# Kernel optimization log

Measured on AMD Instinct MI355X. Metric: run time of the kernel, lower is better.

The kernel has to match this reference:

```python
import jax, jax.numpy as jnp
import numpy as np

B = 2048          # graphs in dense batch
NPG = 64          # nodes per graph (molecules are small)
N = B * NPG       # 131072 total nodes
E = 524288        # directed edges, avg degree 4
D = 275           # dim_inner
L = 5             # layers_mp
NF = 9            # atom categorical features
V = 128           # per-feature vocab
BN_EPS = 1e-5


def setup_inputs() -> dict:
    key = jax.random.key(0)
    ks = jax.random.split(key, 8)
    return {
        "x_atoms": jax.random.randint(ks[0], (N, NF), 0, 119, dtype=jnp.int64),
        "edge_index": jax.random.randint(ks[1], (2, E), 0, N, dtype=jnp.int64),
        "atom_emb": jax.random.normal(ks[2], (NF, V, D), jnp.float32) * 0.1,
        "conv_W": jax.random.normal(ks[3], (L, D, D), jnp.float32) * (1.0 / np.sqrt(D)),
        "conv_b": jnp.zeros((L, D), jnp.float32),
        "bn_gamma": jnp.ones((L, D), jnp.float32),
        "bn_beta": jnp.zeros((L, D), jnp.float32),
        "post_W": jax.random.normal(ks[4], (D, D), jnp.float32) * (1.0 / np.sqrt(D)),
        "post_b": jnp.zeros((D,), jnp.float32),
    }


def reference(x_atoms, edge_index, atom_emb, conv_W, conv_b, bn_gamma, bn_beta, post_W, post_b):
    n = x_atoms.shape[0]
    # AtomEncoder: sum of per-feature embedding lookups -> [N, D]
    h = jax.vmap(lambda tab, idx: tab[idx], in_axes=(0, 1))(atom_emb, x_atoms).sum(0)

    # GCN normalization with self loops (shared across layers since graph is fixed)
    loops = jnp.arange(n, dtype=edge_index.dtype)
    row = jnp.concatenate([edge_index[0], loops])  # source
    col = jnp.concatenate([edge_index[1], loops])  # target (aggregation index)
    deg = jax.ops.segment_sum(jnp.ones_like(row, h.dtype), col, num_segments=n)
    dinv = jnp.where(deg > 0, jax.lax.rsqrt(jnp.maximum(deg, 1e-12)), 0.0)
    norm = dinv[row] * dinv[col]  # [E+N]

    for i in range(L):
        xw = h @ conv_W[i].T                                   # [N, D] linear (no bias yet)
        msg = norm[:, None] * xw[row]                          # gather + edge scaling
        agg = jax.ops.segment_sum(msg, col, num_segments=n) + conv_b[i]
        # BatchNorm1d (training-mode batch stats, biased variance)
        mu = agg.mean(axis=0)
        var = agg.var(axis=0)
        hbn = (agg - mu) * jax.lax.rsqrt(var + BN_EPS) * bn_gamma[i] + bn_beta[i]
        h = jax.nn.relu(hbn)

    # post_mp: single Linear (MLPNoAct, num_layers=1)
    h = h @ post_W.T + post_b

    # graph_preprocess -> dense batch [B, NPG, D], then pairwise dot-product decode
    hd = h.reshape(B, NPG, D)
    logits = jnp.einsum('bnd,bmd->bnm', hd, hd)[..., None]     # [B, NPG, NPG, 1]
    return logits
```

## Files before the change

### kernel.cpp

```cpp
#include <hip/hip_runtime.h>
#include <hip/hip_bf16.h>
#include <cstdint>

#define NN 131072
#define NE 524288
#define DIM 275
#define DP 288
#define NFEAT 9
#define NVOC 128
#define NLAY 5
#define NPG 64
#define NGRAPH 2048
#define BN_EPS 1e-5f
#define BM 128
#define BK 32
#define NEPAD (NE + 3 * NN)
#define LDSE 1536

typedef unsigned short u16;
typedef __attribute__((ext_vector_type(8))) short s16x8;
typedef __attribute__((ext_vector_type(4))) float f32x4;

__device__ __forceinline__ float bf2f(u16 u) {
  union { unsigned int i; float f; } x; x.i = ((unsigned int)u) << 16; return x.f;
}
__device__ __forceinline__ u16 f2bf(float f) {
  union { float f; unsigned int i; } x; x.f = f;
  unsigned int r = x.i + 0x7fffu + ((x.i >> 16) & 1u);
  return (u16)(r >> 16);
}
__device__ __forceinline__ void acc4(float* a, uint2 m) {
  a[0] += bf2f((u16)m.x); a[1] += bf2f((u16)(m.x >> 16));
  a[2] += bf2f((u16)m.y); a[3] += bf2f((u16)(m.y >> 16));
}


__global__ void hist_kernel(const int* __restrict__ ei, int* __restrict__ cnt) {
  int e = blockIdx.x * 256 + threadIdx.x;
  if (e < NE) atomicAdd(&cnt[ei[NE + e]], 1);
}

__global__ void pad_dinv_kernel(const int* __restrict__ cnt, int* __restrict__ cnt_pad,
                                float* __restrict__ dinv) {
  int v = blockIdx.x * 256 + threadIdx.x;
  if (v < NN) {
    int c = cnt[v];
    cnt_pad[v] = (c + 3) & ~3;
    dinv[v] = rsqrtf(1.0f + (float)c);
  }
}

__global__ void scan_block_kernel(const int* __restrict__ in, int* __restrict__ out_ex,
                                  int* __restrict__ partials) {
  __shared__ int buf[2][1024];
  int t = threadIdx.x;
  int idx = blockIdx.x * 1024 + t;
  int v = in[idx];
  buf[0][t] = v;
  __syncthreads();
  int cur = 0;
  for (int off = 1; off < 1024; off <<= 1) {
    int x = buf[cur][t];
    if (t >= off) x += buf[cur][t - off];
    buf[cur ^ 1][t] = x;
    __syncthreads();
    cur ^= 1;
  }
  out_ex[idx] = buf[cur][t] - v;
  if (t == 1023) partials[blockIdx.x] = buf[cur][t];
}

__global__ void scan_partials_kernel(int* partials) {
  __shared__ int buf[2][128];
  int t = threadIdx.x;
  int v = partials[t];
  buf[0][t] = v;
  __syncthreads();
  int cur = 0;
  for (int off = 1; off < 128; off <<= 1) {
    int x = buf[cur][t];
    if (t >= off) x += buf[cur][t - off];
    buf[cur ^ 1][t] = x;
    __syncthreads();
    cur ^= 1;
  }
  partials[t] = buf[cur][t] - v;
}

__global__ void add_offsets_kernel(int* __restrict__ indptr, const int* __restrict__ partials,
                                   int* __restrict__ cursor, const int* __restrict__ cnt_pad) {
  int i = blockIdx.x * 256 + threadIdx.x;
  if (i < NN) {
    int v = indptr[i] + partials[i >> 10];
    indptr[i] = v;
    cursor[i] = v;
    if (i == NN - 1) indptr[NN] = v + cnt_pad[NN - 1];
  }
}

__global__ void fill_csr_kernel(const int* __restrict__ ei, int* __restrict__ cursor,
                                int* __restrict__ srcs) {
  int e = blockIdx.x * 256 + threadIdx.x;
  if (e < NE) {
    int c = ei[NE + e];
    int p = atomicAdd(&cursor[c], 1);
    srcs[p] = ei[e];
  }
}

__global__ void pad_fill_kernel(const int* __restrict__ cursor, const int* __restrict__ indptr,
                                int* __restrict__ srcs) {
  int v = blockIdx.x * 256 + threadIdx.x;
  if (v < NN) {
    int pe = indptr[v + 1];
    for (int p = cursor[v]; p < pe; ++p) srcs[p] = NN;
  }
}

__global__ void zrow_kernel(u16* __restrict__ P, u16* __restrict__ Q) {
  int i = threadIdx.x;
  if (i < DP) {
    P[(size_t)NN * DP + i] = 0;
    Q[(size_t)NN * DP + i] = 0;
  }
}

__global__ void wpad_kernel(const float* __restrict__ convW, const float* __restrict__ postW,
                            u16* __restrict__ Wp) {
  int i = blockIdx.x * 256 + threadIdx.x;
  const int total = 6 * 320 * DP;
  if (i >= total) return;
  int k = i % DP;
  int r = i / DP;
  int j = r % 320;
  int m = r / 320;
  float val = 0.f;
  if (j < DIM && k < DIM)
    val = (m < 5) ? convW[((size_t)m * DIM + j) * DIM + k] : postW[(size_t)j * DIM + k];
  Wp[i] = f2bf(val);
}


__global__ void embed_kernel(const int* __restrict__ xa, const float* __restrict__ emb,
                             u16* __restrict__ P) {
  int n = blockIdx.x;
  int idx[NFEAT];
#pragma unroll
  for (int f = 0; f < NFEAT; ++f) idx[f] = xa[n * NFEAT + f];
  for (int d = threadIdx.x; d < DP; d += 128) {
    float s = 0.f;
    if (d < DIM) {
#pragma unroll
      for (int f = 0; f < NFEAT; ++f) s += emb[((size_t)f * NVOC + idx[f]) * DIM + d];
    }
    P[(size_t)n * DP + d] = f2bf(s);
  }
}


__device__ __forceinline__ uint4 xform8(uint4 r, const float* __restrict__ sc,
                                        const float* __restrict__ sh, int k) {
  union { uint4 u; u16 h[8]; } in, out;
  in.u = r;
#pragma unroll
  for (int j = 0; j < 8; ++j) {
    float x = fmaf(bf2f(in.h[j]), sc[k + j], sh[k + j]);
    out.h[j] = f2bf(fmaxf(x, 0.f));
  }
  return out.u;
}

__launch_bounds__(256)
__global__ void gemm_kernel(const u16* __restrict__ A, const u16* __restrict__ Wp,
                            u16* __restrict__ C,
                            const float* __restrict__ scale, const float* __restrict__ shift,
                            const float* __restrict__ rowscale, const float* __restrict__ colbias) {
  __shared__ __align__(16) u16 Asl[BM * BK];
  __shared__ __align__(16) u16 Bsl[160 * BK];
  const int tid = threadIdx.x;
  const int lane = tid & 63;
  const int wv = tid >> 6, wm = wv & 1, wn = wv >> 1;
  const int b = blockIdx.x;
  const int grp = b >> 4, rem = b & 15;
  const int col = rem >> 3, pan8 = rem & 7;
  const int row0 = (grp * 8 + pan8) * BM, col0 = col * 128;

  const int sr = tid >> 2, ssl = tid & 3;
  const int swz = ((ssl ^ (sr & 3) ^ ((sr >> 2) & 3)) << 3);
  const int aw0 = sr * BK + swz;
  const u16* ag0 = A + (size_t)(row0 + sr) * DP + ssl * 8;
  const u16* ag1 = ag0 + (size_t)64 * DP;
  const u16* bg0 = Wp + (size_t)(col0 + sr) * DP + ssl * 8;
  const u16* bg1 = bg0 + (size_t)64 * DP;
  const u16* bg2 = bg0 + (size_t)128 * DP;
  const bool st2 = (tid < 128);

  const int fr = lane & 15, fs = lane >> 4;
  const int fswz = ((fs ^ (fr & 3) ^ ((fr >> 2) & 3)) << 3);
  int aoff[4], boff[5];
#pragma unroll
  for (int i = 0; i < 4; ++i) aoff[i] = (wm * 64 + i * 16 + fr) * BK + fswz;
#pragma unroll
  for (int j = 0; j < 5; ++j) boff[j] = (wn * 80 + j * 16 + fr) * BK + fswz;

  const bool bn = (scale != nullptr);
  const int NS = DP / BK;

  {
    uint4 ra0 = *(const uint4*)(ag0);
    uint4 ra1 = *(const uint4*)(ag1);
    uint4 rb0 = *(const uint4*)(bg0);
    uint4 rb1 = *(const uint4*)(bg1);
    uint4 rb2;
    if (st2) rb2 = *(const uint4*)(bg2);
    if (bn) {
      ra0 = xform8(ra0, scale, shift, ssl * 8);
      ra1 = xform8(ra1, scale, shift, ssl * 8);
    }
    *(uint4*)&Asl[aw0] = ra0;
    *(uint4*)&Asl[aw0 + 64 * BK] = ra1;
    *(uint4*)&Bsl[aw0] = rb0;
    *(uint4*)&Bsl[aw0 + 64 * BK] = rb1;
    if (st2) *(uint4*)&Bsl[aw0 + 128 * BK] = rb2;
  }
  __syncthreads();

  f32x4 acc[4][5];
#pragma unroll
  for (int i = 0; i < 4; ++i)
#pragma unroll
    for (int j = 0; j < 5; ++j) acc[i][j] = (f32x4){0.f, 0.f, 0.f, 0.f};

  for (int s = 0; s < NS; ++s) {
    const bool more = (s < NS - 1);
    uint4 na0, na1, nb0, nb1, nb2;
    if (more) {
      na0 = *(const uint4*)(ag0 + (s + 1) * BK);
      na1 = *(const uint4*)(ag1 + (s + 1) * BK);
      nb0 = *(const uint4*)(bg0 + (s + 1) * BK);
      nb1 = *(const uint4*)(bg1 + (s + 1) * BK);
      if (st2) nb2 = *(const uint4*)(bg2 + (s + 1) * BK);
    }
    s16x8 af[4], bf[5];
#pragma unroll
    for (int i = 0; i < 4; ++i) af[i] = *(const s16x8*)&Asl[aoff[i]];
#pragma unroll
    for (int j = 0; j < 5; ++j) bf[j] = *(const s16x8*)&Bsl[boff[j]];
#pragma unroll
    for (int i = 0; i < 4; ++i)
#pragma unroll
      for (int j = 0; j < 5; ++j)
        acc[i][j] = __builtin_amdgcn_mfma_f32_16x16x32_bf16(af[i], bf[j], acc[i][j], 0, 0, 0);
    if (more) {
      __syncthreads();
      int k2 = (s + 1) * BK + ssl * 8;
      if (bn) {
        na0 = xform8(na0, scale, shift, k2);
        na1 = xform8(na1, scale, shift, k2);
      }
      *(uint4*)&Asl[aw0] = na0;
      *(uint4*)&Asl[aw0 + 64 * BK] = na1;
      *(uint4*)&Bsl[aw0] = nb0;
      *(uint4*)&Bsl[aw0 + 64 * BK] = nb1;
      if (st2) *(uint4*)&Bsl[aw0 + 128 * BK] = nb2;
      __syncthreads();
    }
  }

#pragma unroll
  for (int i = 0; i < 4; ++i) {
    int gr0 = row0 + wm * 64 + i * 16 + fs * 4;
    float rs[4];
#pragma unroll
    for (int r = 0; r < 4; ++r) rs[r] = rowscale ? rowscale[gr0 + r] : 1.f;
#pragma unroll
    for (int j = 0; j < 5; ++j) {
      int gc = col0 + wn * 80 + j * 16 + fr;
      if (gc < DP) {
        float cb = (colbias && gc < DIM) ? colbias[gc] : 0.f;
#pragma unroll
        for (int r = 0; r < 4; ++r) {
          u16 o = (gc < DIM) ? f2bf(fmaf(acc[i][j][r], rs[r], cb)) : (u16)0;
          C[(size_t)(gr0 + r) * DP + gc] = o;
        }
      }
    }
  }
}


__launch_bounds__(256)
__global__ void spmm_kernel(const u16* __restrict__ X, u16* __restrict__ Y,
                            const int* __restrict__ indptr, const int* __restrict__ srcs,
                            const float* __restrict__ dinv, const float* __restrict__ bias,
                            float* __restrict__ bn_sum, float* __restrict__ bn_sq) {
  __shared__ float ls[DP], lq[DP];
  __shared__ int sptr[65];
  __shared__ int sidx[LDSE];
  int tid = threadIdx.x;
  for (int i = tid; i < DP; i += 256) { ls[i] = 0.f; lq[i] = 0.f; }
  int vb = blockIdx.x * 64;
  if (tid < 65) sptr[tid] = indptr[vb + tid];
  __syncthreads();
  int ebase = sptr[0];
  int ecnt = sptr[64] - ebase;
  const int* ip;
  if (ecnt <= LDSE) {
    for (int i = tid; i < ecnt; i += 256) sidx[i] = srcs[ebase + i];
    ip = sidx;
  } else {
    ip = srcs + ebase;
  }
  __syncthreads();

  int lane = tid & 63, wv = tid >> 6;
  int c0 = lane << 2;
  int c1 = 256 + (lane << 2);
  bool tl = lane < 8;
  float bia[4], bib[4];
#pragma unroll
  for (int j = 0; j < 4; ++j) bia[j] = bias[c0 + j];
#pragma unroll
  for (int j = 0; j < 4; ++j) bib[j] = (tl && c1 + j < DIM) ? bias[c1 + j] : 0.f;
  float s0[4] = {}, q0[4] = {}, s1[4] = {}, q1[4] = {};

  for (int g = 0; g < 8; ++g) {
    int nA = wv * 16 + g;
    int nB = nA + 8;
    int ebA = sptr[nA] - ebase, neA = sptr[nA + 1] - sptr[nA];
    int ebB = sptr[nB] - ebase, neB = sptr[nB + 1] - sptr[nB];
    int nemax = neA > neB ? neA : neB;
    const u16* xA = X + (size_t)(vb + nA) * DP;
    const u16* xB = X + (size_t)(vb + nB) * DP;
    uint2 mA = *(const uint2*)(xA + c0);
    uint2 mB = *(const uint2*)(xB + c0);
    uint2 tA, tB;
    if (tl) { tA = *(const uint2*)(xA + c1); tB = *(const uint2*)(xB + c1); }
    float A0[4] = {}, B0[4] = {}, A1[4] = {}, B1[4] = {};
    acc4(A0, mA); acc4(B0, mB);
    if (tl) { acc4(A1, tA); acc4(B1, tB); }

    for (int e = 0; e < nemax; e += 4) {
      bool aA = e < neA, aB = e < neB;
      int oA = aA ? ebA + e : 0;
      int oB = aB ? ebB + e : 0;
      int ia[4], ib[4];
#pragma unroll
      for (int j = 0; j < 4; ++j) {
        int va = ip[oA + j], vbx = ip[oB + j];
        ia[j] = aA ? va : NN;
        ib[j] = aB ? vbx : NN;
      }
      const u16* pa[4]; const u16* pb[4];
#pragma unroll
      for (int j = 0; j < 4; ++j) {
        pa[j] = X + (size_t)ia[j] * DP;
        pb[j] = X + (size_t)ib[j] * DP;
      }
      uint2 ma[4], mb[4];
#pragma unroll
      for (int j = 0; j < 4; ++j) ma[j] = *(const uint2*)(pa[j] + c0);
#pragma unroll
      for (int j = 0; j < 4; ++j) mb[j] = *(const uint2*)(pb[j] + c0);
      uint2 ta[4], tb[4];
      if (tl) {
#pragma unroll
        for (int j = 0; j < 4; ++j) ta[j] = *(const uint2*)(pa[j] + c1);
#pragma unroll
        for (int j = 0; j < 4; ++j) tb[j] = *(const uint2*)(pb[j] + c1);
      }
#pragma unroll
      for (int j = 0; j < 4; ++j) { acc4(A0, ma[j]); acc4(B0, mb[j]); }
      if (tl) {
#pragma unroll
        for (int j = 0; j < 4; ++j) { acc4(A1, ta[j]); acc4(B1, tb[j]); }
      }
    }

    float dvA = dinv[vb + nA], dvB = dinv[vb + nB];
    u16* yA = Y + (size_t)(vb + nA) * DP;
    u16* yB = Y + (size_t)(vb + nB) * DP;
    float ya[4], yb[4];
#pragma unroll
    for (int j = 0; j < 4; ++j) {
      ya[j] = fmaf(dvA, A0[j], bia[j]);
      s0[j] += ya[j]; q0[j] += ya[j] * ya[j];
      yb[j] = fmaf(dvB, B0[j], bia[j]);
      s0[j] += yb[j]; q0[j] += yb[j] * yb[j];
    }
    uint2 wa, wb;
    wa.x = (unsigned)f2bf(ya[0]) | ((unsigned)f2bf(ya[1]) << 16);
    wa.y = (unsigned)f2bf(ya[2]) | ((unsigned)f2bf(ya[3]) << 16);
    wb.x = (unsigned)f2bf(yb[0]) | ((unsigned)f2bf(yb[1]) << 16);
    wb.y = (unsigned)f2bf(yb[2]) | ((unsigned)f2bf(yb[3]) << 16);
    *(uint2*)(yA + c0) = wa;
    *(uint2*)(yB + c0) = wb;
    if (tl) {
      float za[4], zb[4];
#pragma unroll
      for (int j = 0; j < 4; ++j) {
        za[j] = fmaf(dvA, A1[j], bib[j]);
        s1[j] += za[j]; q1[j] += za[j] * za[j];
        zb[j] = fmaf(dvB, B1[j], bib[j]);
        s1[j] += zb[j]; q1[j] += zb[j] * zb[j];
      }
      uint2 ua, ub;
      ua.x = (unsigned)f2bf(za[0]) | ((unsigned)f2bf(za[1]) << 16);
      ua.y = (unsigned)f2bf(za[2]) | ((unsigned)f2bf(za[3]) << 16);
      ub.x = (unsigned)f2bf(zb[0]) | ((unsigned)f2bf(zb[1]) << 16);
      ub.y = (unsigned)f2bf(zb[2]) | ((unsigned)f2bf(zb[3]) << 16);
      *(uint2*)(yA + c1) = ua;
      *(uint2*)(yB + c1) = ub;
    }
  }

#pragma unroll
  for (int j = 0; j < 4; ++j) { atomicAdd(&ls[c0 + j], s0[j]); atomicAdd(&lq[c0 + j], q0[j]); }
  if (tl) {
#pragma unroll
    for (int j = 0; j < 4; ++j) { atomicAdd(&ls[c1 + j], s1[j]); atomicAdd(&lq[c1 + j], q1[j]); }
  }
  __syncthreads();
  for (int i = tid; i < DP; i += 256) {
    atomicAdd(&bn_sum[i], ls[i]);
    atomicAdd(&bn_sq[i], lq[i]);
  }
}

__global__ void bn_finalize_kernel(const float* __restrict__ bn_sum, const float* __restrict__ bn_sq,
                                   const float* __restrict__ gamma, const float* __restrict__ beta,
                                   float* __restrict__ scale, float* __restrict__ shift) {
  int d = threadIdx.x;
  if (d >= DP) return;
  if (d < DIM) {
    const float invN = 1.0f / (float)NN;
    float mu = bn_sum[d] * invN;
    float var = bn_sq[d] * invN - mu * mu;
    float rstd = rsqrtf(var + BN_EPS);
    float sc = gamma[d] * rstd;
    scale[d] = sc;
    shift[d] = fmaf(-mu, sc, beta[d]);
  } else {
    scale[d] = 0.f;
    shift[d] = 0.f;
  }
}


__launch_bounds__(256)
__global__ void decode_kernel(const u16* __restrict__ H, float* __restrict__ out) {
  __shared__ __align__(16) u16 tile[4][2][NPG * BK];
  int tid = threadIdx.x, lane = tid & 63, wv = tid >> 6;
  int g = blockIdx.x * 4 + wv;
  const u16* Hg = H + (size_t)g * NPG * DP;
  const int ssl = lane & 3;
  int soff[4];
  const u16* sg[4];
#pragma unroll
  for (int i = 0; i < 4; ++i) {
    int r = (lane >> 2) + i * 16;
    soff[i] = r * BK + ((ssl ^ (r & 3) ^ ((r >> 2) & 3)) << 3);
    sg[i] = Hg + (size_t)r * DP + ssl * 8;
  }
  const int fr = lane & 15, fs = lane >> 4;
  const int fswz = ((fs ^ (fr & 3) ^ ((fr >> 2) & 3)) << 3);
  int foff[4];
#pragma unroll
  for (int i = 0; i < 4; ++i) foff[i] = (i * 16 + fr) * BK + fswz;

  u16* t0 = tile[wv][0];
  u16* t1 = tile[wv][1];
  uint4 rg[4];
#pragma unroll
  for (int i = 0; i < 4; ++i) rg[i] = *(const uint4*)(sg[i]);
#pragma unroll
  for (int i = 0; i < 4; ++i) *(uint4*)&t0[soff[i]] = rg[i];

  f32x4 acc[4][4];
#pragma unroll
  for (int i = 0; i < 4; ++i)
#pragma unroll
    for (int j = 0; j < 4; ++j) acc[i][j] = (f32x4){0.f, 0.f, 0.f, 0.f};

  for (int s = 0; s < DP / BK; ++s) {
    u16* cur = (s & 1) ? t1 : t0;
    u16* nxt = (s & 1) ? t0 : t1;
    const bool more = (s < DP / BK - 1);
    if (more) {
#pragma unroll
      for (int i = 0; i < 4; ++i) rg[i] = *(const uint4*)(sg[i] + (s + 1) * BK);
    }
    s16x8 af[4];
#pragma unroll
    for (int i = 0; i < 4; ++i) af[i] = *(const s16x8*)&cur[foff[i]];
#pragma unroll
    for (int i = 0; i < 4; ++i)
#pragma unroll
      for (int j = 0; j < 4; ++j)
        acc[i][j] = __builtin_amdgcn_mfma_f32_16x16x32_bf16(af[i], af[j], acc[i][j], 0, 0, 0);
    if (more) {
#pragma unroll
      for (int i = 0; i < 4; ++i) *(uint4*)&nxt[soff[i]] = rg[i];
    }
  }
  float* og = out + (size_t)g * NPG * NPG;
#pragma unroll
  for (int i = 0; i < 4; ++i) {
    int m0 = i * 16 + fs * 4;
#pragma unroll
    for (int j = 0; j < 4; ++j) {
      int n = j * 16 + fr;
#pragma unroll
      for (int r = 0; r < 4; ++r) og[(m0 + r) * NPG + n] = acc[i][j][r];
    }
  }
}


extern "C" void kernel_launch(void* const* d_in, const int* in_sizes, int n_in,
                              void* d_out, int out_size, void* d_ws, size_t ws_size,
                              hipStream_t stream) {
  const int* xa = (const int*)d_in[0];
  const int* ei = (const int*)d_in[1];
  const float* emb = (const float*)d_in[2];
  const float* convW = (const float*)d_in[3];
  const float* convB = (const float*)d_in[4];
  const float* gamma = (const float*)d_in[5];
  const float* beta = (const float*)d_in[6];
  const float* postW = (const float*)d_in[7];
  const float* postB = (const float*)d_in[8];
  float* out = (float*)d_out;

  char* w = (char*)d_ws;
  u16* P = (u16*)w;          w += (size_t)(NN + 1) * DP * sizeof(u16);
  u16* Q = (u16*)w;          w += (size_t)(NN + 1) * DP * sizeof(u16);
  u16* Wp = (u16*)w;         w += (size_t)6 * 320 * DP * sizeof(u16);
  float* dinv = (float*)w;   w += (size_t)NN * sizeof(float);
  int* cnt = (int*)w;        w += (size_t)NN * sizeof(int);
  int* cnt_pad = (int*)w;    w += (size_t)NN * sizeof(int);
  int* indptr = (int*)w;     w += (size_t)(NN + 64) * sizeof(int);
  int* cursor = (int*)w;     w += (size_t)NN * sizeof(int);
  int* srcs = (int*)w;       w += (size_t)NEPAD * sizeof(int);
  int* partials = (int*)w;   w += 256 * sizeof(int);
  float* bn_sum = (float*)w; w += DP * sizeof(float);
  float* bn_sq = (float*)w;  w += DP * sizeof(float);
  float* bnscale = (float*)w; w += DP * sizeof(float);
  float* bnshift = (float*)w; w += DP * sizeof(float);

  size_t need = (size_t)(w - (char*)d_ws);
  if (ws_size < need) return;

  hipMemsetAsync(cnt, 0, (size_t)NN * sizeof(int), stream);
  hist_kernel<<<NE / 256, 256, 0, stream>>>(ei, cnt);
  pad_dinv_kernel<<<NN / 256, 256, 0, stream>>>(cnt, cnt_pad, dinv);
  scan_block_kernel<<<NN / 1024, 1024, 0, stream>>>(cnt_pad, indptr, partials);
  scan_partials_kernel<<<1, 128, 0, stream>>>(partials);
  add_offsets_kernel<<<NN / 256, 256, 0, stream>>>(indptr, partials, cursor, cnt_pad);
  fill_csr_kernel<<<NE / 256, 256, 0, stream>>>(ei, cursor, srcs);
  pad_fill_kernel<<<NN / 256, 256, 0, stream>>>(cursor, indptr, srcs);
  wpad_kernel<<<(6 * 320 * DP + 255) / 256, 256, 0, stream>>>(convW, postW, Wp);
  embed_kernel<<<NN, 128, 0, stream>>>(xa, emb, P);
  zrow_kernel<<<1, 288, 0, stream>>>(P, Q);

  for (int l = 0; l < NLAY; ++l) {
    gemm_kernel<<<(NN / BM) * 2, 256, 0, stream>>>(
        P, Wp + (size_t)l * 320 * DP, Q,
        l ? bnscale : nullptr, l ? bnshift : nullptr, dinv, nullptr);
    hipMemsetAsync(bn_sum, 0, 2 * DP * sizeof(float), stream);
    spmm_kernel<<<NN / 64, 256, 0, stream>>>(Q, P, indptr, srcs, dinv,
                                             convB + (size_t)l * DIM, bn_sum, bn_sq);
    bn_finalize_kernel<<<1, DP, 0, stream>>>(bn_sum, bn_sq, gamma + (size_t)l * DIM,
                                             beta + (size_t)l * DIM, bnscale, bnshift);
  }

  gemm_kernel<<<(NN / BM) * 2, 256, 0, stream>>>(
      P, Wp + (size_t)5 * 320 * DP, Q, bnscale, bnshift, nullptr, postB);

  decode_kernel<<<NGRAPH / 4, 256, 0, stream>>>(Q, out);
}
```

Before: 1.093 ms.

## Restructure GEMM so each block computes full output width with A in registers

The GEMM now gives each block 128 rows across all 288 output columns. Each wave keeps its 32-row A fragments in registers, loaded straight from global memory, and streams the whole weight matrix through a double-buffered, padded LDS tile with one barrier per K step. This removes the 2x column split, which re-read A and recomputed the BN transform twice, and drops the A staging through LDS. The cost is 144 accumulator registers per thread, which can lower occupancy, and uncoalesced per-lane A loads.

```diff
diff --git a/kernel.cpp b/kernel.cpp
--- a/kernel.cpp
+++ b/kernel.cpp
@@ -12,7 +12,6 @@
 #define NPG 64
 #define NGRAPH 2048
 #define BN_EPS 1e-5f
-#define BM 128
 #define BK 32
 #define NEPAD (NE + 3 * NN)
 #define LDSE 1536
@@ -175,114 +174,90 @@
                             u16* __restrict__ C,
                             const float* __restrict__ scale, const float* __restrict__ shift,
                             const float* __restrict__ rowscale, const float* __restrict__ colbias) {
-  __shared__ __align__(16) u16 Asl[BM * BK];
-  __shared__ __align__(16) u16 Bsl[160 * BK];
-  const int tid = threadIdx.x;
-  const int lane = tid & 63;
-  const int wv = tid >> 6, wm = wv & 1, wn = wv >> 1;
-  const int b = blockIdx.x;
-  const int grp = b >> 4, rem = b & 15;
-  const int col = rem >> 3, pan8 = rem & 7;
-  const int row0 = (grp * 8 + pan8) * BM, col0 = col * 128;
-
-  const int sr = tid >> 2, ssl = tid & 3;
-  const int swz = ((ssl ^ (sr & 3) ^ ((sr >> 2) & 3)) << 3);
-  const int aw0 = sr * BK + swz;
-  const u16* ag0 = A + (size_t)(row0 + sr) * DP + ssl * 8;
-  const u16* ag1 = ag0 + (size_t)64 * DP;
-  const u16* bg0 = Wp + (size_t)(col0 + sr) * DP + ssl * 8;
-  const u16* bg1 = bg0 + (size_t)64 * DP;
-  const u16* bg2 = bg0 + (size_t)128 * DP;
-  const bool st2 = (tid < 128);
-
-  const int fr = lane & 15, fs = lane >> 4;
-  const int fswz = ((fs ^ (fr & 3) ^ ((fr >> 2) & 3)) << 3);
-  int aoff[4], boff[5];
-#pragma unroll
-  for (int i = 0; i < 4; ++i) aoff[i] = (wm * 64 + i * 16 + fr) * BK + fswz;
-#pragma unroll
-  for (int j = 0; j < 5; ++j) boff[j] = (wn * 80 + j * 16 + fr) * BK + fswz;
-
+  __shared__ __align__(16) u16 Bs[2][320 * 40];
+  const int tid = threadIdx.x, lane = tid & 63, wv = tid >> 6;
+  const int lr = lane & 15, lk = lane >> 4;
+  const int row0 = blockIdx.x * 128 + wv * 32;
+  const u16* ag0 = A + (size_t)(row0 + lr) * DP + lk * 8;
+  const u16* ag1 = ag0 + (size_t)16 * DP;
+  const int srow = tid >> 2, schk = tid & 3;
+  const u16* sg = Wp + (size_t)srow * DP + schk * 8;
+  const int swoff = srow * 40 + schk * 8;
+  const int bbase = lr * 40 + lk * 8;
   const bool bn = (scale != nullptr);
-  const int NS = DP / BK;
-
-  {
-    uint4 ra0 = *(const uint4*)(ag0);
-    uint4 ra1 = *(const uint4*)(ag1);
-    uint4 rb0 = *(const uint4*)(bg0);
-    uint4 rb1 = *(const uint4*)(bg1);
-    uint4 rb2;
-    if (st2) rb2 = *(const uint4*)(bg2);
+
+#pragma unroll
+  for (int i = 0; i < 5; ++i) {
+    uint4 rb = *(const uint4*)(sg + (size_t)(64 * i) * DP);
+    *(uint4*)&Bs[0][swoff + 64 * i * 40] = rb;
+  }
+  uint4 a0 = *(const uint4*)(ag0);
+  uint4 a1 = *(const uint4*)(ag1);
+  __syncthreads();
+
+  f32x4 acc0[18], acc1[18];
+#pragma unroll
+  for (int j = 0; j < 18; ++j) {
+    acc0[j] = (f32x4){0.f, 0.f, 0.f, 0.f};
+    acc1[j] = (f32x4){0.f, 0.f, 0.f, 0.f};
+  }
+
+#pragma unroll 1
+  for (int s = 0; s < 9; ++s) {
+    const bool more = (s < 8);
+    uint4 n0, n1, nb0, nb1, nb2, nb3, nb4;
+    if (more) {
+      int k = (s + 1) * BK;
+      nb0 = *(const uint4*)(sg + k);
+      nb1 = *(const uint4*)(sg + (size_t)64 * DP + k);
+      nb2 = *(const uint4*)(sg + (size_t)128 * DP + k);
+      nb3 = *(const uint4*)(sg + (size_t)192 * DP + k);
+      nb4 = *(const uint4*)(sg + (size_t)256 * DP + k);
+      n0 = *(const uint4*)(ag0 + k);
+      n1 = *(const uint4*)(ag1 + k);
+    }
     if (bn) {
-      ra0 = xform8(ra0, scale, shift, ssl * 8);
-      ra1 = xform8(ra1, scale, shift, ssl * 8);
-    }
-    *(uint4*)&Asl[aw0] = ra0;
-    *(uint4*)&Asl[aw0 + 64 * BK] = ra1;
-    *(uint4*)&Bsl[aw0] = rb0;
-    *(uint4*)&Bsl[aw0 + 64 * BK] = rb1;
-    if (st2) *(uint4*)&Bsl[aw0 + 128 * BK] = rb2;
-  }
-  __syncthreads();
-
-  f32x4 acc[4][5];
-#pragma unroll
-  for (int i = 0; i < 4; ++i)
-#pragma unroll
-    for (int j = 0; j < 5; ++j) acc[i][j] = (f32x4){0.f, 0.f, 0.f, 0.f};
-
-  for (int s = 0; s < NS; ++s) {
-    const bool more = (s < NS - 1);
-    uint4 na0, na1, nb0, nb1, nb2;
+      int kk = s * BK + lk * 8;
+      a0 = xform8(a0, scale, shift, kk);
+      a1 = xform8(a1, scale, shift, kk);
+    }
+    union { uint4 u; s16x8 v; } ca, cb;
+    ca.u = a0; s16x8 af0 = ca.v;
+    cb.u = a1; s16x8 af1 = cb.v;
+    const u16* bp = &Bs[s & 1][bbase];
+#pragma unroll
+    for (int j = 0; j < 18; ++j) {
+      s16x8 bf = *(const s16x8*)&bp[j * 640];
+      acc0[j] = __builtin_amdgcn_mfma_f32_16x16x32_bf16(af0, bf, acc0[j], 0, 0, 0);
+      acc1[j] = __builtin_amdgcn_mfma_f32_16x16x32_bf16(af1, bf, acc1[j], 0, 0, 0);
+    }
     if (more) {
-      na0 = *(const uint4*)(ag0 + (s + 1) * BK);
-      na1 = *(const uint4*)(ag1 + (s + 1) * BK);
-      nb0 = *(const uint4*)(bg0 + (s + 1) * BK);
-      nb1 = *(const uint4*)(bg1 + (s + 1) * BK);
-      if (st2) nb2 = *(const uint4*)(bg2 + (s + 1) * BK);
-    }
-    s16x8 af[4], bf[5];
-#pragma unroll
-    for (int i = 0; i < 4; ++i) af[i] = *(const s16x8*)&Asl[aoff[i]];
-#pragma unroll
-    for (int j = 0; j < 5; ++j) bf[j] = *(const s16x8*)&Bsl[boff[j]];
-#pragma unroll
-    for (int i = 0; i < 4; ++i)
-#pragma unroll
-      for (int j = 0; j < 5; ++j)
-        acc[i][j] = __builtin_amdgcn_mfma_f32_16x16x32_bf16(af[i], bf[j], acc[i][j], 0, 0, 0);
-    if (more) {
-      __syncthreads();
-      int k2 = (s + 1) * BK + ssl * 8;
-      if (bn) {
-        na0 = xform8(na0, scale, shift, k2);
-        na1 = xform8(na1, scale, shift, k2);
-      }
-      *(uint4*)&Asl[aw0] = na0;
-      *(uint4*)&Asl[aw0 + 64 * BK] = na1;
-      *(uint4*)&Bsl[aw0] = nb0;
-      *(uint4*)&Bsl[aw0 + 64 * BK] = nb1;
-      if (st2) *(uint4*)&Bsl[aw0 + 128 * BK] = nb2;
-      __syncthreads();
-    }
-  }
-
-#pragma unroll
-  for (int i = 0; i < 4; ++i) {
-    int gr0 = row0 + wm * 64 + i * 16 + fs * 4;
+      u16* bq = &Bs[(s + 1) & 1][swoff];
+      *(uint4*)&bq[0] = nb0;
+      *(uint4*)&bq[64 * 40] = nb1;
+      *(uint4*)&bq[128 * 40] = nb2;
+      *(uint4*)&bq[192 * 40] = nb3;
+      *(uint4*)&bq[256 * 40] = nb4;
+      a0 = n0; a1 = n1;
+    }
+    __syncthreads();
+  }
+
+#pragma unroll
+  for (int i = 0; i < 2; ++i) {
+    int gr0 = row0 + i * 16 + lk * 4;
     float rs[4];
 #pragma unroll
     for (int r = 0; r < 4; ++r) rs[r] = rowscale ? rowscale[gr0 + r] : 1.f;
 #pragma unroll
-    for (int j = 0; j < 5; ++j) {
-      int gc = col0 + wn * 80 + j * 16 + fr;
-      if (gc < DP) {
-        float cb = (colbias && gc < DIM) ? colbias[gc] : 0.f;
-#pragma unroll
-        for (int r = 0; r < 4; ++r) {
-          u16 o = (gc < DIM) ? f2bf(fmaf(acc[i][j][r], rs[r], cb)) : (u16)0;
-          C[(size_t)(gr0 + r) * DP + gc] = o;
-        }
+    for (int j = 0; j < 18; ++j) {
+      f32x4 av = i ? acc1[j] : acc0[j];
+      int gc = j * 16 + lr;
+      float cb = (colbias && gc < DIM) ? colbias[gc] : 0.f;
+#pragma unroll
+      for (int r = 0; r < 4; ++r) {
+        u16 o = (gc < DIM) ? f2bf(fmaf(av[r], rs[r], cb)) : (u16)0;
+        C[(size_t)(gr0 + r) * DP + gc] = o;
       }
     }
   }
@@ -563,7 +538,7 @@
   zrow_kernel<<<1, 288, 0, stream>>>(P, Q);
 
   for (int l = 0; l < NLAY; ++l) {
-    gemm_kernel<<<(NN / BM) * 2, 256, 0, stream>>>(
+    gemm_kernel<<<NN / 128, 256, 0, stream>>>(
         P, Wp + (size_t)l * 320 * DP, Q,
         l ? bnscale : nullptr, l ? bnshift : nullptr, dinv, nullptr);
     hipMemsetAsync(bn_sum, 0, 2 * DP * sizeof(float), stream);
@@ -573,7 +548,7 @@
                                              beta + (size_t)l * DIM, bnscale, bnshift);
   }
 
-  gemm_kernel<<<(NN / BM) * 2, 256, 0, stream>>>(
+  gemm_kernel<<<NN / 128, 256, 0, stream>>>(
       P, Wp + (size_t)5 * 320 * DP, Q, bnscale, bnshift, nullptr, postB);
 
   decode_kernel<<<NGRAPH / 4, 256, 0, stream>>>(Q, out);
```

After: 1.217 ms. 1.11x slower.
